# Kernel optimization log

Hardware: AMD Instinct MI355X
Metric: run time of the kernel (lower is better)

Reference implementation:

```python
import jax, jax.numpy as jnp
import numpy as np

B, N, E, EA = 4, 100000, 160000, 80000
HID, ED = 128, 16

def _xavier(key, fan_in, fan_out):
    lim = float(np.sqrt(6.0 / (fan_in + fan_out)))
    return jax.random.uniform(key, (fan_in, fan_out), jnp.float32, -lim, lim)

def setup_inputs() -> dict:
    key = jax.random.key(0)
    k1, k2, k3, k4, k5, k6 = jax.random.split(key, 6)
    h = jax.random.normal(k1, (B, N, HID), jnp.float32)
    edge_index = jax.random.randint(k2, (2, E), 0, N, jnp.int64)
    edge_attr = jax.random.normal(k3, (B, E, ED), jnp.float32)
    # index-array equivalent of the boolean edge_type_mask (even count EA)
    edge_type_idx = jnp.sort(jax.random.randint(k4, (EA,), 0, E, jnp.int64))
    d_in = 2 * HID + ED
    W1 = _xavier(k5, d_in, HID)
    b1 = jnp.zeros((HID,), jnp.float32)
    W2 = _xavier(k6, HID, 2)
    b2 = jnp.zeros((2,), jnp.float32)
    return {"h": h, "edge_index": edge_index, "edge_attr": edge_attr,
            "edge_type_idx": edge_type_idx, "W1": W1, "b1": b1, "W2": W2, "b2": b2}

def reference(h, edge_index, edge_attr, edge_type_idx, W1, b1, W2, b2):
    # gather only the masked edges (same math as gather-all then mask)
    sel_r = edge_index[0][edge_type_idx]   # [EA]
    sel_s = edge_index[1][edge_type_idx]   # [EA]
    h_received_a = h[:, sel_r, :]          # [B, EA, HID]
    h_sent_a = h[:, sel_s, :]              # [B, EA, HID]
    edge_attr_a = edge_attr[:, edge_type_idx, :]  # [B, EA, ED]
    x = jnp.concatenate([h_received_a, h_sent_a, edge_attr_a], axis=-1)
    x = jax.nn.relu(jnp.einsum('bef,fh->beh', x, W1) + b1)
    out = jnp.einsum('beh,ho->beo', x, W2) + b2      # [B, EA, 2]
    b, ea, o = out.shape
    return out.reshape(b, ea // 2, 2, o).mean(axis=2)  # [B, EA//2, 2]
```

## Files before the change

kernel.cpp:

```cpp
#include <hip/hip_runtime.h>
#include <hip/hip_bf16.h>

#define NB 4
#define N_NODES 100000
#define E_EDGES 160000
#define EA_E 80000
#define HID 128
#define ED 16

#define TILE_M 128
#define THREADS 256
#define XPAD 40

typedef __attribute__((ext_vector_type(8))) short bf16x8;
typedef __attribute__((ext_vector_type(4))) float f32x4;
typedef __attribute__((ext_vector_type(8))) unsigned short u16x8;

__device__ __forceinline__ unsigned short f2bf(float f) {
    union { __hip_bfloat16 b; unsigned short u; } v;
    v.b = __float2bfloat16(f);
    return v.u;
}

__device__ __forceinline__ void gll16(const void* g, void* l) {
    __builtin_amdgcn_global_load_lds(
        (const __attribute__((address_space(1))) unsigned int*)g,
        (__attribute__((address_space(3))) unsigned int*)l, 16, 0, 0);
}

__global__ void prep_w1(const float* __restrict__ W1, unsigned short* __restrict__ W1F) {
    const int cb   = blockIdx.x;
    const int c    = cb >> 3;
    const int ni   = cb & 7;
    const int lane = threadIdx.x;
    const int fr   = lane & 15;
    const int fq   = lane >> 4;
    const int n    = ni * 16 + fr;
    u16x8 v;
    #pragma unroll
    for (int j = 0; j < 8; ++j) {
        int k = c * 32 + fq * 8 + j;
        float f = (k < 272) ? W1[(size_t)k * HID + n] : 0.f;
        v[j] = f2bf(f);
    }
    *reinterpret_cast<u16x8*>(W1F + ((size_t)(cb * 64 + lane)) * 8) = v;
}

__global__ __launch_bounds__(THREADS, 3) void actor_head_mfma(
    const float* __restrict__ h,
    const int*   __restrict__ edge_index,
    const float* __restrict__ edge_attr,
    const int*   __restrict__ etype,
    const unsigned short* __restrict__ W1F,
    const float* __restrict__ b1,
    const float* __restrict__ W2,
    const float* __restrict__ b2,
    float*       __restrict__ out)
{
    __shared__ unsigned short xs[2][TILE_M][XPAD];
    __shared__ unsigned short bws[2][4096];
    __shared__ int sel[3][TILE_M];

    const int b  = blockIdx.y;
    const int e0 = blockIdx.x * TILE_M;
    const int t  = threadIdx.x;

    if (t < TILE_M) {
        int ei = etype[e0 + t];
        sel[2][t] = ei;
        sel[0][t] = edge_index[ei];
        sel[1][t] = edge_index[E_EDGES + ei];
    }

    const int lane = t & 63;
    const int wid  = t >> 6;
    const int wm   = wid * 32;
    const int fr   = lane & 15;
    const int fq   = lane >> 4;

    const int sm = t >> 1;
    const int sh = t & 1;

    f32x4 tv[4];
    f32x4 acc[2][8];
    #pragma unroll
    for (int i = 0; i < 2; ++i)
        #pragma unroll
        for (int j = 0; j < 8; ++j) acc[i][j] = (f32x4){0.f, 0.f, 0.f, 0.f};

    __syncthreads();

    const float* hr = h + ((size_t)b * N_NODES + sel[0][sm]) * HID + sh * 16;
    const float* hs = h + ((size_t)b * N_NODES + sel[1][sm]) * HID + sh * 16;
    const float* ea = edge_attr + ((size_t)b * E_EDGES + sel[2][sm]) * ED;

#define GATHER(cn) do { if ((cn) <= 8) { \
    if ((cn) < 8) { \
        const float* q = (((cn) < 4) ? hr : hs) + ((cn) & 3) * 32; \
        tv[0] = *reinterpret_cast<const f32x4*>(q); \
        tv[1] = *reinterpret_cast<const f32x4*>(q + 4); \
        tv[2] = *reinterpret_cast<const f32x4*>(q + 8); \
        tv[3] = *reinterpret_cast<const f32x4*>(q + 12); \
    } else if (sh == 0) { \
        tv[0] = *reinterpret_cast<const f32x4*>(ea); \
        tv[1] = *reinterpret_cast<const f32x4*>(ea + 4); \
        tv[2] = *reinterpret_cast<const f32x4*>(ea + 8); \
        tv[3] = *reinterpret_cast<const f32x4*>(ea + 12); \
    } else { \
        tv[0] = tv[1] = tv[2] = tv[3] = (f32x4){0.f, 0.f, 0.f, 0.f}; \
    } } } while (0)

#define DMA_B(cn) do { if ((cn) <= 8) { \
    _Pragma("unroll") \
    for (int j2 = 0; j2 < 2; ++j2) \
        gll16(W1F + (size_t)(((cn) * 8 + j2 * 4 + wid) * 64 + lane) * 8, \
              &bws[(cn) & 1][(j2 * 4 + wid) * 512]); } } while (0)

#define CVT_STAGE(buf) do { u16x8 lo_, hi_; \
    _Pragma("unroll") \
    for (int j = 0; j < 4; ++j) { \
        lo_[j]     = f2bf(tv[0][j]); lo_[4 + j] = f2bf(tv[1][j]); \
        hi_[j]     = f2bf(tv[2][j]); hi_[4 + j] = f2bf(tv[3][j]); } \
    *reinterpret_cast<u16x8*>(&xs[(buf)][sm][sh * 16 + 0]) = lo_; \
    *reinterpret_cast<u16x8*>(&xs[(buf)][sm][sh * 16 + 8]) = hi_; } while (0)

#define MFMA_C(c) do { bf16x8 af0_, af1_; \
    af0_ = *reinterpret_cast<const bf16x8*>(&xs[(c) & 1][wm + fr][fq * 8]); \
    af1_ = *reinterpret_cast<const bf16x8*>(&xs[(c) & 1][wm + 16 + fr][fq * 8]); \
    _Pragma("unroll") \
    for (int ni = 0; ni < 8; ++ni) { \
        bf16x8 bw_ = *reinterpret_cast<const bf16x8*>(&bws[(c) & 1][ni * 512 + lane * 8]); \
        acc[0][ni] = __builtin_amdgcn_mfma_f32_16x16x32_bf16(af0_, bw_, acc[0][ni], 0, 0, 0); \
        acc[1][ni] = __builtin_amdgcn_mfma_f32_16x16x32_bf16(af1_, bw_, acc[1][ni], 0, 0, 0); } } while (0)

    DMA_B(0);
    __builtin_amdgcn_sched_barrier(0);
    GATHER(0);
    CVT_STAGE(0);
    GATHER(1);
    __builtin_amdgcn_sched_barrier(0);
    asm volatile("s_waitcnt vmcnt(4) lgkmcnt(0)" ::: "memory");
    __builtin_amdgcn_sched_barrier(0);
    __builtin_amdgcn_s_barrier();

    for (int c = 0; c < 8; ++c) {
        DMA_B(c + 1);
        __builtin_amdgcn_sched_barrier(0);
        CVT_STAGE((c + 1) & 1);
        GATHER(c + 2);
        MFMA_C(c);
        __builtin_amdgcn_sched_barrier(0);
        if (c < 6) {
            asm volatile("s_waitcnt vmcnt(4) lgkmcnt(0)" ::: "memory");
        } else {
            asm volatile("s_waitcnt vmcnt(0) lgkmcnt(0)" ::: "memory");
        }
        __builtin_amdgcn_sched_barrier(0);
        __builtin_amdgcn_s_barrier();
    }
    MFMA_C(8);

    float b1v[8], w2a[8], w2b[8];
    #pragma unroll
    for (int ni = 0; ni < 8; ++ni) {
        int n = ni * 16 + fr;
        b1v[ni] = b1[n];
        w2a[ni] = W2[2 * n + 0];
        w2b[ni] = W2[2 * n + 1];
    }
    const float b20 = b2[0], b21 = b2[1];

    #pragma unroll
    for (int mi = 0; mi < 2; ++mi) {
        #pragma unroll
        for (int j = 0; j < 2; ++j) {
            float s0 = 0.f, s1 = 0.f;
            #pragma unroll
            for (int ni = 0; ni < 8; ++ni) {
                float y0 = fmaxf(acc[mi][ni][2 * j]     + b1v[ni], 0.f);
                float y1 = fmaxf(acc[mi][ni][2 * j + 1] + b1v[ni], 0.f);
                float ys = y0 + y1;
                s0 = fmaf(ys, w2a[ni], s0);
                s1 = fmaf(ys, w2b[ni], s1);
            }
            #pragma unroll
            for (int off = 8; off >= 1; off >>= 1) {
                s0 += __shfl_xor(s0, off);
                s1 += __shfl_xor(s1, off);
            }
            if (fr == 0) {
                int mg = e0 + wm + mi * 16 + fq * 4 + 2 * j;
                size_t oi = ((size_t)b * (EA_E / 2) + (mg >> 1)) * 2;
                out[oi + 0] = 0.5f * s0 + b20;
                out[oi + 1] = 0.5f * s1 + b21;
            }
        }
    }
}

extern "C" void kernel_launch(void* const* d_in, const int* in_sizes, int n_in,
                              void* d_out, int out_size, void* d_ws, size_t ws_size,
                              hipStream_t stream) {
    const float* h          = (const float*)d_in[0];
    const int*   edge_index = (const int*)d_in[1];
    const float* edge_attr  = (const float*)d_in[2];
    const int*   etype      = (const int*)d_in[3];
    const float* W1         = (const float*)d_in[4];
    const float* b1         = (const float*)d_in[5];
    const float* W2         = (const float*)d_in[6];
    const float* b2         = (const float*)d_in[7];
    float* out = (float*)d_out;

    unsigned short* W1F = (unsigned short*)d_ws;

    prep_w1<<<72, 64, 0, stream>>>(W1, W1F);

    dim3 grid(EA_E / TILE_M, NB);
    actor_head_mfma<<<grid, THREADS, 0, stream>>>(
        h, edge_index, edge_attr, etype, W1F, b1, W2, b2, out);
}
```

Baseline: 57.82 us.

## Gather A fragments directly into MFMA registers, removing LDS staging

```diff
diff --git a/kernel.cpp b/kernel.cpp
--- a/kernel.cpp
+++ b/kernel.cpp
@@ -10,7 +10,6 @@
 
 #define TILE_M 128
 #define THREADS 256
-#define XPAD 40
 
 typedef __attribute__((ext_vector_type(8))) short bf16x8;
 typedef __attribute__((ext_vector_type(4))) float f32x4;
@@ -20,6 +19,15 @@
     union { __hip_bfloat16 b; unsigned short u; } v;
     v.b = __float2bfloat16(f);
     return v.u;
+}
+
+__device__ __forceinline__ bf16x8 cvt8(f32x4 a, f32x4 c) {
+    bf16x8 r;
+    r[0] = (short)f2bf(a[0]); r[1] = (short)f2bf(a[1]);
+    r[2] = (short)f2bf(a[2]); r[3] = (short)f2bf(a[3]);
+    r[4] = (short)f2bf(c[0]); r[5] = (short)f2bf(c[1]);
+    r[6] = (short)f2bf(c[2]); r[7] = (short)f2bf(c[3]);
+    return r;
 }
 
 __device__ __forceinline__ void gll16(const void* g, void* l) {
@@ -57,7 +65,6 @@
     const float* __restrict__ b2,
     float*       __restrict__ out)
 {
-    __shared__ unsigned short xs[2][TILE_M][XPAD];
     __shared__ unsigned short bws[2][4096];
     __shared__ int sel[3][TILE_M];
 
@@ -78,10 +85,7 @@
     const int fr   = lane & 15;
     const int fq   = lane >> 4;
 
-    const int sm = t >> 1;
-    const int sh = t & 1;
-
-    f32x4 tv[4];
+    f32x4 tvA[4], tvB[4];
     f32x4 acc[2][8];
     #pragma unroll
     for (int i = 0; i < 2; ++i)
@@ -90,24 +94,29 @@
 
     __syncthreads();
 
-    const float* hr = h + ((size_t)b * N_NODES + sel[0][sm]) * HID + sh * 16;
-    const float* hs = h + ((size_t)b * N_NODES + sel[1][sm]) * HID + sh * 16;
-    const float* ea = edge_attr + ((size_t)b * E_EDGES + sel[2][sm]) * ED;
-
-#define GATHER(cn) do { if ((cn) <= 8) { \
+    const int r0 = wm + fr, r1 = wm + 16 + fr;
+    const float* pr0 = h + ((size_t)b * N_NODES + sel[0][r0]) * HID;
+    const float* pr1 = h + ((size_t)b * N_NODES + sel[0][r1]) * HID;
+    const float* ps0 = h + ((size_t)b * N_NODES + sel[1][r0]) * HID;
+    const float* ps1 = h + ((size_t)b * N_NODES + sel[1][r1]) * HID;
+    const float* pe0 = edge_attr + ((size_t)b * E_EDGES + sel[2][r0]) * ED;
+    const float* pe1 = edge_attr + ((size_t)b * E_EDGES + sel[2][r1]) * ED;
+
+#define GATHER(TV, cn) do { if ((cn) <= 8) { \
     if ((cn) < 8) { \
-        const float* q = (((cn) < 4) ? hr : hs) + ((cn) & 3) * 32; \
-        tv[0] = *reinterpret_cast<const f32x4*>(q); \
-        tv[1] = *reinterpret_cast<const f32x4*>(q + 4); \
-        tv[2] = *reinterpret_cast<const f32x4*>(q + 8); \
-        tv[3] = *reinterpret_cast<const f32x4*>(q + 12); \
-    } else if (sh == 0) { \
-        tv[0] = *reinterpret_cast<const f32x4*>(ea); \
-        tv[1] = *reinterpret_cast<const f32x4*>(ea + 4); \
-        tv[2] = *reinterpret_cast<const f32x4*>(ea + 8); \
-        tv[3] = *reinterpret_cast<const f32x4*>(ea + 12); \
+        const float* q0 = (((cn) < 4) ? pr0 : ps0) + ((cn) & 3) * 32 + fq * 8; \
+        const float* q1 = (((cn) < 4) ? pr1 : ps1) + ((cn) & 3) * 32 + fq * 8; \
+        TV[0] = *reinterpret_cast<const f32x4*>(q0); \
+        TV[1] = *reinterpret_cast<const f32x4*>(q0 + 4); \
+        TV[2] = *reinterpret_cast<const f32x4*>(q1); \
+        TV[3] = *reinterpret_cast<const f32x4*>(q1 + 4); \
+    } else if (fq < 2) { \
+        TV[0] = *reinterpret_cast<const f32x4*>(pe0 + fq * 8); \
+        TV[1] = *reinterpret_cast<const f32x4*>(pe0 + fq * 8 + 4); \
+        TV[2] = *reinterpret_cast<const f32x4*>(pe1 + fq * 8); \
+        TV[3] = *reinterpret_cast<const f32x4*>(pe1 + fq * 8 + 4); \
     } else { \
-        tv[0] = tv[1] = tv[2] = tv[3] = (f32x4){0.f, 0.f, 0.f, 0.f}; \
+        TV[0] = TV[1] = TV[2] = TV[3] = (f32x4){0.f, 0.f, 0.f, 0.f}; \
     } } } while (0)
 
 #define DMA_B(cn) do { if ((cn) <= 8) { \
@@ -116,49 +125,48 @@
         gll16(W1F + (size_t)(((cn) * 8 + j2 * 4 + wid) * 64 + lane) * 8, \
               &bws[(cn) & 1][(j2 * 4 + wid) * 512]); } } while (0)
 
-#define CVT_STAGE(buf) do { u16x8 lo_, hi_; \
-    _Pragma("unroll") \
-    for (int j = 0; j < 4; ++j) { \
-        lo_[j]     = f2bf(tv[0][j]); lo_[4 + j] = f2bf(tv[1][j]); \
-        hi_[j]     = f2bf(tv[2][j]); hi_[4 + j] = f2bf(tv[3][j]); } \
-    *reinterpret_cast<u16x8*>(&xs[(buf)][sm][sh * 16 + 0]) = lo_; \
-    *reinterpret_cast<u16x8*>(&xs[(buf)][sm][sh * 16 + 8]) = hi_; } while (0)
-
-#define MFMA_C(c) do { bf16x8 af0_, af1_; \
-    af0_ = *reinterpret_cast<const bf16x8*>(&xs[(c) & 1][wm + fr][fq * 8]); \
-    af1_ = *reinterpret_cast<const bf16x8*>(&xs[(c) & 1][wm + 16 + fr][fq * 8]); \
+#define MFMA_ACC(c, AF0, AF1) do { \
     _Pragma("unroll") \
     for (int ni = 0; ni < 8; ++ni) { \
         bf16x8 bw_ = *reinterpret_cast<const bf16x8*>(&bws[(c) & 1][ni * 512 + lane * 8]); \
-        acc[0][ni] = __builtin_amdgcn_mfma_f32_16x16x32_bf16(af0_, bw_, acc[0][ni], 0, 0, 0); \
-        acc[1][ni] = __builtin_amdgcn_mfma_f32_16x16x32_bf16(af1_, bw_, acc[1][ni], 0, 0, 0); } } while (0)
-
+        acc[0][ni] = __builtin_amdgcn_mfma_f32_16x16x32_bf16(AF0, bw_, acc[0][ni], 0, 0, 0); \
+        acc[1][ni] = __builtin_amdgcn_mfma_f32_16x16x32_bf16(AF1, bw_, acc[1][ni], 0, 0, 0); } } while (0)
+
+#define PH(c, TV, VMN) do { \
+    DMA_B((c) + 1); \
+    __builtin_amdgcn_sched_barrier(0); \
+    bf16x8 af0_ = cvt8(TV[0], TV[1]); \
+    bf16x8 af1_ = cvt8(TV[2], TV[3]); \
+    GATHER(TV, (c) + 2); \
+    __builtin_amdgcn_sched_barrier(0); \
+    MFMA_ACC(c, af0_, af1_); \
+    __builtin_amdgcn_sched_barrier(0); \
+    asm volatile("s_waitcnt vmcnt(" #VMN ")" ::: "memory"); \
+    __builtin_amdgcn_sched_barrier(0); \
+    __builtin_amdgcn_s_barrier(); } while (0)
+
+    GATHER(tvA, 0);
     DMA_B(0);
     __builtin_amdgcn_sched_barrier(0);
-    GATHER(0);
-    CVT_STAGE(0);
-    GATHER(1);
+    GATHER(tvB, 1);
     __builtin_amdgcn_sched_barrier(0);
-    asm volatile("s_waitcnt vmcnt(4) lgkmcnt(0)" ::: "memory");
+    asm volatile("s_waitcnt vmcnt(4)" ::: "memory");
     __builtin_amdgcn_sched_barrier(0);
     __builtin_amdgcn_s_barrier();
 
-    for (int c = 0; c < 8; ++c) {
-        DMA_B(c + 1);
-        __builtin_amdgcn_sched_barrier(0);
-        CVT_STAGE((c + 1) & 1);
-        GATHER(c + 2);
-        MFMA_C(c);
-        __builtin_amdgcn_sched_barrier(0);
-        if (c < 6) {
-            asm volatile("s_waitcnt vmcnt(4) lgkmcnt(0)" ::: "memory");
-        } else {
-            asm volatile("s_waitcnt vmcnt(0) lgkmcnt(0)" ::: "memory");
-        }
-        __builtin_amdgcn_sched_barrier(0);
-        __builtin_amdgcn_s_barrier();
-    }
-    MFMA_C(8);
+    PH(0, tvA, 4);
+    PH(1, tvB, 4);
+    PH(2, tvA, 4);
+    PH(3, tvB, 4);
+    PH(4, tvA, 4);
+    PH(5, tvB, 4);
+    PH(6, tvA, 4);
+    PH(7, tvB, 0);
+    {
+        bf16x8 af8a = cvt8(tvA[0], tvA[1]);
+        bf16x8 af8b = cvt8(tvA[2], tvA[3]);
+        MFMA_ACC(8, af8a, af8b);
+    }
 
     float b1v[8], w2a[8], w2b[8];
     #pragma unroll
```

After: 64.61 us. +11.7%, slower.

## Deepen gather/weight prefetch pipeline to three stages with double register buffers

Applied to the files above, without the earlier changes.

```diff
diff --git a/kernel.cpp b/kernel.cpp
--- a/kernel.cpp
+++ b/kernel.cpp
@@ -58,7 +58,7 @@
     float*       __restrict__ out)
 {
     __shared__ unsigned short xs[2][TILE_M][XPAD];
-    __shared__ unsigned short bws[2][4096];
+    __shared__ unsigned short bws[3][4096];
     __shared__ int sel[3][TILE_M];
 
     const int b  = blockIdx.y;
@@ -81,7 +81,7 @@
     const int sm = t >> 1;
     const int sh = t & 1;
 
-    f32x4 tv[4];
+    f32x4 tvA[4], tvB[4];
     f32x4 acc[2][8];
     #pragma unroll
     for (int i = 0; i < 2; ++i)
@@ -94,33 +94,33 @@
     const float* hs = h + ((size_t)b * N_NODES + sel[1][sm]) * HID + sh * 16;
     const float* ea = edge_attr + ((size_t)b * E_EDGES + sel[2][sm]) * ED;
 
-#define GATHER(cn) do { if ((cn) <= 8) { \
+#define GATHER(TV, cn) do { if ((cn) <= 8) { \
     if ((cn) < 8) { \
         const float* q = (((cn) < 4) ? hr : hs) + ((cn) & 3) * 32; \
-        tv[0] = *reinterpret_cast<const f32x4*>(q); \
-        tv[1] = *reinterpret_cast<const f32x4*>(q + 4); \
-        tv[2] = *reinterpret_cast<const f32x4*>(q + 8); \
-        tv[3] = *reinterpret_cast<const f32x4*>(q + 12); \
+        TV[0] = *reinterpret_cast<const f32x4*>(q); \
+        TV[1] = *reinterpret_cast<const f32x4*>(q + 4); \
+        TV[2] = *reinterpret_cast<const f32x4*>(q + 8); \
+        TV[3] = *reinterpret_cast<const f32x4*>(q + 12); \
     } else if (sh == 0) { \
-        tv[0] = *reinterpret_cast<const f32x4*>(ea); \
-        tv[1] = *reinterpret_cast<const f32x4*>(ea + 4); \
-        tv[2] = *reinterpret_cast<const f32x4*>(ea + 8); \
-        tv[3] = *reinterpret_cast<const f32x4*>(ea + 12); \
+        TV[0] = *reinterpret_cast<const f32x4*>(ea); \
+        TV[1] = *reinterpret_cast<const f32x4*>(ea + 4); \
+        TV[2] = *reinterpret_cast<const f32x4*>(ea + 8); \
+        TV[3] = *reinterpret_cast<const f32x4*>(ea + 12); \
     } else { \
-        tv[0] = tv[1] = tv[2] = tv[3] = (f32x4){0.f, 0.f, 0.f, 0.f}; \
+        TV[0] = TV[1] = TV[2] = TV[3] = (f32x4){0.f, 0.f, 0.f, 0.f}; \
     } } } while (0)
 
 #define DMA_B(cn) do { if ((cn) <= 8) { \
     _Pragma("unroll") \
     for (int j2 = 0; j2 < 2; ++j2) \
         gll16(W1F + (size_t)(((cn) * 8 + j2 * 4 + wid) * 64 + lane) * 8, \
-              &bws[(cn) & 1][(j2 * 4 + wid) * 512]); } } while (0)
-
-#define CVT_STAGE(buf) do { u16x8 lo_, hi_; \
+              &bws[(cn) % 3][(j2 * 4 + wid) * 512]); } } while (0)
+
+#define CVT_STAGE(TV, buf) do { u16x8 lo_, hi_; \
     _Pragma("unroll") \
     for (int j = 0; j < 4; ++j) { \
-        lo_[j]     = f2bf(tv[0][j]); lo_[4 + j] = f2bf(tv[1][j]); \
-        hi_[j]     = f2bf(tv[2][j]); hi_[4 + j] = f2bf(tv[3][j]); } \
+        lo_[j]     = f2bf(TV[0][j]); lo_[4 + j] = f2bf(TV[1][j]); \
+        hi_[j]     = f2bf(TV[2][j]); hi_[4 + j] = f2bf(TV[3][j]); } \
     *reinterpret_cast<u16x8*>(&xs[(buf)][sm][sh * 16 + 0]) = lo_; \
     *reinterpret_cast<u16x8*>(&xs[(buf)][sm][sh * 16 + 8]) = hi_; } while (0)
 
@@ -129,35 +129,42 @@
     af1_ = *reinterpret_cast<const bf16x8*>(&xs[(c) & 1][wm + 16 + fr][fq * 8]); \
     _Pragma("unroll") \
     for (int ni = 0; ni < 8; ++ni) { \
-        bf16x8 bw_ = *reinterpret_cast<const bf16x8*>(&bws[(c) & 1][ni * 512 + lane * 8]); \
+        bf16x8 bw_ = *reinterpret_cast<const bf16x8*>(&bws[(c) % 3][ni * 512 + lane * 8]); \
         acc[0][ni] = __builtin_amdgcn_mfma_f32_16x16x32_bf16(af0_, bw_, acc[0][ni], 0, 0, 0); \
         acc[1][ni] = __builtin_amdgcn_mfma_f32_16x16x32_bf16(af1_, bw_, acc[1][ni], 0, 0, 0); } } while (0)
 
+#define PH(c, TV, VMN) do { \
+    DMA_B((c) + 2); \
+    __builtin_amdgcn_sched_barrier(0); \
+    CVT_STAGE(TV, ((c) + 1) & 1); \
+    GATHER(TV, (c) + 3); \
+    __builtin_amdgcn_sched_barrier(0); \
+    MFMA_C(c); \
+    __builtin_amdgcn_sched_barrier(0); \
+    asm volatile("s_waitcnt vmcnt(" #VMN ") lgkmcnt(0)" ::: "memory"); \
+    __builtin_amdgcn_sched_barrier(0); \
+    __builtin_amdgcn_s_barrier(); } while (0)
+
+    GATHER(tvA, 0);
     DMA_B(0);
+    GATHER(tvB, 1);
+    DMA_B(1);
     __builtin_amdgcn_sched_barrier(0);
-    GATHER(0);
-    CVT_STAGE(0);
-    GATHER(1);
+    CVT_STAGE(tvA, 0);
+    GATHER(tvA, 2);
     __builtin_amdgcn_sched_barrier(0);
-    asm volatile("s_waitcnt vmcnt(4) lgkmcnt(0)" ::: "memory");
+    asm volatile("s_waitcnt vmcnt(10) lgkmcnt(0)" ::: "memory");
     __builtin_amdgcn_sched_barrier(0);
     __builtin_amdgcn_s_barrier();
 
-    for (int c = 0; c < 8; ++c) {
-        DMA_B(c + 1);
-        __builtin_amdgcn_sched_barrier(0);
-        CVT_STAGE((c + 1) & 1);
-        GATHER(c + 2);
-        MFMA_C(c);
-        __builtin_amdgcn_sched_barrier(0);
-        if (c < 6) {
-            asm volatile("s_waitcnt vmcnt(4) lgkmcnt(0)" ::: "memory");
-        } else {
-            asm volatile("s_waitcnt vmcnt(0) lgkmcnt(0)" ::: "memory");
-        }
-        __builtin_amdgcn_sched_barrier(0);
-        __builtin_amdgcn_s_barrier();
-    }
+    PH(0, tvB, 10);
+    PH(1, tvA, 10);
+    PH(2, tvB, 10);
+    PH(3, tvA, 10);
+    PH(4, tvB, 10);
+    PH(5, tvA, 10);
+    PH(6, tvB, 6);
+    PH(7, tvA, 0);
     MFMA_C(8);
 
     float b1v[8], w2a[8], w2b[8];
```

New measurement: 61.24 us. +5.9%, slower.
